# Kernel optimization log

Hardware: AMD Instinct MI355X
Metric: run time of the kernel (lower is better)

## Reference

```python
import jax, jax.numpy as jnp
import numpy as np

HID = 1280
CROSS = 2048
HEAD_DIM = 64
N_HEADS = HID // HEAD_DIM  # 20
FF = 4 * HID               # 5120
EPS = 1e-5


def _layernorm(x, g, b):
    mu = jnp.mean(x, axis=-1, keepdims=True)
    var = jnp.mean(jnp.square(x - mu), axis=-1, keepdims=True)
    return (x - mu) * jax.lax.rsqrt(var + EPS) * g + b


def _attention(x_q, x_kv, wq, wk, wv, wo, bo):
    b, t, _ = x_q.shape
    q = x_q @ wq.T  # [b,t,HID]
    k = x_kv @ wk.T
    v = x_kv @ wv.T
    q = q.reshape(b, t, N_HEADS, HEAD_DIM).transpose(0, 2, 1, 3)
    s = x_kv.shape[1]
    k = k.reshape(b, s, N_HEADS, HEAD_DIM).transpose(0, 2, 1, 3)
    v = v.reshape(b, s, N_HEADS, HEAD_DIM).transpose(0, 2, 1, 3)
    scale = HEAD_DIM ** -0.5
    scores = jnp.einsum('bhtd,bhsd->bhts', q, k) * scale
    attn = jax.nn.softmax(scores, axis=-1)
    o = jnp.einsum('bhts,bhsd->bhtd', attn, v)
    o = o.transpose(0, 2, 1, 3).reshape(b, t, HID)
    return o @ wo.T + bo


def setup_inputs() -> dict:
    key = jax.random.key(0)
    ks = jax.random.split(key, 16)
    std = 0.02
    d = {}
    d['x'] = jax.random.normal(ks[0], (2, 2048, HID), jnp.float32)
    d['encoder_hidden_states'] = jax.random.normal(ks[1], (2, 77, CROSS), jnp.float32)
    d['ln1_g'] = jnp.ones((HID,), jnp.float32); d['ln1_b'] = jnp.zeros((HID,), jnp.float32)
    d['ln2_g'] = jnp.ones((HID,), jnp.float32); d['ln2_b'] = jnp.zeros((HID,), jnp.float32)
    d['ln3_g'] = jnp.ones((HID,), jnp.float32); d['ln3_b'] = jnp.zeros((HID,), jnp.float32)
    d['wq1'] = jax.random.normal(ks[2], (HID, HID), jnp.float32) * std
    d['wk1'] = jax.random.normal(ks[3], (HID, HID), jnp.float32) * std
    d['wv1'] = jax.random.normal(ks[4], (HID, HID), jnp.float32) * std
    d['wo1'] = jax.random.normal(ks[5], (HID, HID), jnp.float32) * std
    d['bo1'] = jnp.zeros((HID,), jnp.float32)
    d['wq2'] = jax.random.normal(ks[6], (HID, HID), jnp.float32) * std
    d['wk2'] = jax.random.normal(ks[7], (HID, CROSS), jnp.float32) * std
    d['wv2'] = jax.random.normal(ks[8], (HID, CROSS), jnp.float32) * std
    d['wo2'] = jax.random.normal(ks[9], (HID, HID), jnp.float32) * std
    d['bo2'] = jnp.zeros((HID,), jnp.float32)
    d['w_geglu'] = jax.random.normal(ks[10], (2 * FF, HID), jnp.float32) * std
    d['b_geglu'] = jnp.zeros((2 * FF,), jnp.float32)
    d['w_ffout'] = jax.random.normal(ks[11], (HID, FF), jnp.float32) * std
    d['b_ffout'] = jnp.zeros((HID,), jnp.float32)
    return d


def reference(x, encoder_hidden_states,
              ln1_g, ln1_b, ln2_g, ln2_b, ln3_g, ln3_b,
              wq1, wk1, wv1, wo1, bo1,
              wq2, wk2, wv2, wo2, bo2,
              w_geglu, b_geglu, w_ffout, b_ffout):
    # self-attention
    h = _layernorm(x, ln1_g, ln1_b)
    x = x + _attention(h, h, wq1, wk1, wv1, wo1, bo1)
    # cross-attention
    h = _layernorm(x, ln2_g, ln2_b)
    x = x + _attention(h, encoder_hidden_states, wq2, wk2, wv2, wo2, bo2)
    # GEGLU feed-forward
    h = _layernorm(x, ln3_g, ln3_b)
    proj = h @ w_geglu.T + b_geglu  # [b,t,2*FF]
    x1, x2 = proj[..., :FF], proj[..., FF:]
    ff = (x1 * jax.nn.gelu(x2, approximate=False)) @ w_ffout.T + b_ffout
    return x + ff
```

## Files before the change

kernel.cpp:

```cpp
#include <hip/hip_runtime.h>

typedef unsigned short u16;
typedef __bf16 bf16x8 __attribute__((ext_vector_type(8)));
typedef float f32x4 __attribute__((ext_vector_type(4)));

#define HID 1280
#define NHEADS 20
#define FFD 5120

__device__ __forceinline__ u16 f2b(float f) {
  union { float f; unsigned u; } a; a.f = f;
  unsigned r = a.u + 0x7FFFu + ((a.u >> 16) & 1u);
  return (u16)(r >> 16);
}

__device__ __forceinline__ float gelu_fast(float x) {
  float z = 1.5957691216f * (x + 0.044715f * x * x * x);
  return x / (1.0f + __expf(-z));
}

__device__ __forceinline__ void g2lds16(const void* g, void* l) {
  __builtin_amdgcn_global_load_lds(
      (__attribute__((address_space(1))) void*)(g),
      (__attribute__((address_space(3))) void*)(l), 16, 0, 0);
}

__device__ __forceinline__ void swz(int& bx, int& by) {
  int nx = gridDim.x, ny = gridDim.y;
  int id = blockIdx.y * nx + blockIdx.x;
  int sx = ((nx & 7) == 0) ? 8 : (((nx & 3) == 0) ? 4 : (((nx & 1) == 0) ? 2 : 1));
  int sy = ((ny & 7) == 0) ? 8 : (((ny & 3) == 0) ? 4 : (((ny & 1) == 0) ? 2 : 1));
  int per = sx * sy;
  int st = id / per, w = id - st * per;
  int nsx = nx / sx;
  int stx = st % nsx, sty = st / nsx;
  bx = stx * sx + (w % sx);
  by = sty * sy + (w / sx);
}

struct CvtArgs {
  const float* src[10];
  u16* dst[10];
  int cum4[11];
};

__global__ __launch_bounds__(256) void cvt_weights(CvtArgs a, int total4) {
  int i = blockIdx.x * 256 + threadIdx.x;
  if (i >= total4) return;
  int seg = 0;
#pragma unroll
  for (int s = 1; s < 10; s++) seg += (i >= a.cum4[s]);
  int j = (i - a.cum4[seg]) * 4;
  float4 f = *(const float4*)(a.src[seg] + j);
  union { unsigned long long u; u16 s[4]; } o;
  o.s[0] = f2b(f.x); o.s[1] = f2b(f.y); o.s[2] = f2b(f.z); o.s[3] = f2b(f.w);
  *(unsigned long long*)(a.dst[seg] + j) = o.u;
}

__global__ __launch_bounds__(256) void cvt_enc(const float* __restrict__ enc,
                                               u16* __restrict__ encp) {
  int i = blockIdx.x * 256 + threadIdx.x;
  int j = i * 4;
  int row = j >> 11;
  unsigned long long out = 0ull;
  if (row < 154) {
    float4 f = *(const float4*)(enc + j);
    union { unsigned long long u; u16 s[4]; } o;
    o.s[0] = f2b(f.x); o.s[1] = f2b(f.y); o.s[2] = f2b(f.z); o.s[3] = f2b(f.w);
    out = o.u;
  }
  *(unsigned long long*)(encp + j) = out;
}

__global__ __launch_bounds__(256) void ln_bf16(const float* __restrict__ X,
                                               const float* __restrict__ g,
                                               const float* __restrict__ bta,
                                               u16* __restrict__ Out) {
  const int row = blockIdx.x, tid = threadIdx.x;
  const float* xr = X + (size_t)row * HID;
  float v[5];
#pragma unroll
  for (int i = 0; i < 5; i++) v[i] = xr[tid + i * 256];
  float s = v[0] + v[1] + v[2] + v[3] + v[4];
#pragma unroll
  for (int off = 32; off >= 1; off >>= 1) s += __shfl_down(s, off);
  __shared__ float red[4];
  if ((tid & 63) == 0) red[tid >> 6] = s;
  __syncthreads();
  float mu = (red[0] + red[1] + red[2] + red[3]) * (1.0f / HID);
  float d = 0.f;
#pragma unroll
  for (int i = 0; i < 5; i++) { float t = v[i] - mu; d += t * t; }
#pragma unroll
  for (int off = 32; off >= 1; off >>= 1) d += __shfl_down(d, off);
  __syncthreads();
  if ((tid & 63) == 0) red[tid >> 6] = d;
  __syncthreads();
  float rstd = rsqrtf((red[0] + red[1] + red[2] + red[3]) * (1.0f / HID) + 1e-5f);
#pragma unroll
  for (int i = 0; i < 5; i++) {
    int c = tid + i * 256;
    Out[(size_t)row * HID + c] = f2b((v[i] - mu) * rstd * g[c] + bta[c]);
  }
}

__global__ __launch_bounds__(256) void gemm_bt(
    const u16* __restrict__ A, const u16* __restrict__ Bw,
    u16* __restrict__ Cb, float* __restrict__ Cf,
    const float* __restrict__ bias, const float* __restrict__ resid,
    int M, int N, int K, int mode, int nsplit) {
  __shared__ u16 As[8192];
  __shared__ u16 Bs[8192];
  const int tid = threadIdx.x;
  const int wid = tid >> 6, lane = tid & 63;
  const int quad = lane >> 4, l16 = lane & 15;
  int bx, by; swz(bx, by);
  const int bm = by * 128, bn = bx * 128;
  const int wm = (wid & 1) * 64, wn = (wid >> 1) * 64;

  size_t aoff[4], boff[4];
#pragma unroll
  for (int c = 0; c < 4; ++c) {
    int g = c * 256 + tid;
    int row = g >> 3, pg = g & 7;
    int sc = (pg ^ (row & 7)) * 8;
    aoff[c] = (size_t)(bm + row) * K + sc;
    boff[c] = (size_t)(bn + row) * K + sc;
  }

  f32x4 acc[4][4] = {};
  const int s7 = l16 & 7;

  for (int k0 = 0; k0 < K; k0 += 64) {
    __syncthreads();
#pragma unroll
    for (int c = 0; c < 4; ++c) {
      g2lds16(A + aoff[c] + k0, &As[(c * 256 + wid * 64) * 8]);
      g2lds16(Bw + boff[c] + k0, &Bs[(c * 256 + wid * 64) * 8]);
    }
    __syncthreads();
#pragma unroll
    for (int kc = 0; kc < 2; kc++) {
      const int ph = ((kc << 2) + quad) ^ s7;
      bf16x8 af[4], bfr[4];
#pragma unroll
      for (int mt = 0; mt < 4; mt++)
        af[mt] = *(const bf16x8*)&As[(wm + mt * 16 + l16) * 64 + ph * 8];
#pragma unroll
      for (int nt = 0; nt < 4; nt++)
        bfr[nt] = *(const bf16x8*)&Bs[(wn + nt * 16 + l16) * 64 + ph * 8];
#pragma unroll
      for (int mt = 0; mt < 4; mt++)
#pragma unroll
        for (int nt = 0; nt < 4; nt++)
          acc[mt][nt] = __builtin_amdgcn_mfma_f32_16x16x32_bf16(af[mt], bfr[nt], acc[mt][nt], 0, 0, 0);
    }
  }

  if (mode == 0) {
#pragma unroll
    for (int mt = 0; mt < 4; mt++)
#pragma unroll
      for (int nt = 0; nt < 4; nt++)
#pragma unroll
        for (int r = 0; r < 4; r++) {
          int row = bm + wm + mt * 16 + quad * 4 + r;
          int col = bn + wn + nt * 16 + l16;
          u16 val = f2b(acc[mt][nt][r]);
          if (nsplit > 0) {
            int t = (col >= 2 * nsplit) ? 2 : ((col >= nsplit) ? 1 : 0);
            int dc = col - t * nsplit;
            Cb[(size_t)t * M * nsplit + (size_t)row * nsplit + dc] = val;
          } else {
            Cb[(size_t)row * N + col] = val;
          }
        }
  } else {
#pragma unroll
    for (int mt = 0; mt < 4; mt++)
#pragma unroll
      for (int nt = 0; nt < 4; nt++)
#pragma unroll
        for (int r = 0; r < 4; r++) {
          int row = bm + wm + mt * 16 + quad * 4 + r;
          int col = bn + wn + nt * 16 + l16;
          size_t idx = (size_t)row * N + col;
          Cf[idx] = acc[mt][nt][r] + bias[col] + resid[idx];
        }
  }
}

__global__ __launch_bounds__(256) void gemm_geglu(
    const u16* __restrict__ A, const u16* __restrict__ W,
    const float* __restrict__ bias, u16* __restrict__ Out,
    int M, int K) {
  __shared__ u16 As[8192];
  __shared__ u16 B1s[4096];
  __shared__ u16 B2s[4096];
  const int tid = threadIdx.x;
  const int wid = tid >> 6, lane = tid & 63;
  const int quad = lane >> 4, l16 = lane & 15;
  int bx, by; swz(bx, by);
  const int bm = by * 128, bn = bx * 64;
  const int wm = (wid & 1) * 64, wn = (wid >> 1) * 32;

  size_t aoff[4], b1off[2], b2off[2];
#pragma unroll
  for (int c = 0; c < 4; ++c) {
    int g = c * 256 + tid;
    int row = g >> 3, pg = g & 7;
    int sc = (pg ^ (row & 7)) * 8;
    aoff[c] = (size_t)(bm + row) * K + sc;
    if (c < 2) {
      b1off[c] = (size_t)(bn + row) * K + sc;
      b2off[c] = (size_t)(FFD + bn + row) * K + sc;
    }
  }

  f32x4 acc1[4][2] = {};
  f32x4 acc2[4][2] = {};
  const int s7 = l16 & 7;

  for (int k0 = 0; k0 < K; k0 += 64) {
    __syncthreads();
#pragma unroll
    for (int c = 0; c < 4; ++c)
      g2lds16(A + aoff[c] + k0, &As[(c * 256 + wid * 64) * 8]);
#pragma unroll
    for (int c = 0; c < 2; ++c) {
      g2lds16(W + b1off[c] + k0, &B1s[(c * 256 + wid * 64) * 8]);
      g2lds16(W + b2off[c] + k0, &B2s[(c * 256 + wid * 64) * 8]);
    }
    __syncthreads();
#pragma unroll
    for (int kc = 0; kc < 2; kc++) {
      const int ph = ((kc << 2) + quad) ^ s7;
      bf16x8 af[4], b1[2], b2[2];
#pragma unroll
      for (int mt = 0; mt < 4; mt++)
        af[mt] = *(const bf16x8*)&As[(wm + mt * 16 + l16) * 64 + ph * 8];
#pragma unroll
      for (int nt = 0; nt < 2; nt++) {
        b1[nt] = *(const bf16x8*)&B1s[(wn + nt * 16 + l16) * 64 + ph * 8];
        b2[nt] = *(const bf16x8*)&B2s[(wn + nt * 16 + l16) * 64 + ph * 8];
      }
#pragma unroll
      for (int mt = 0; mt < 4; mt++)
#pragma unroll
        for (int nt = 0; nt < 2; nt++) {
          acc1[mt][nt] = __builtin_amdgcn_mfma_f32_16x16x32_bf16(af[mt], b1[nt], acc1[mt][nt], 0, 0, 0);
          acc2[mt][nt] = __builtin_amdgcn_mfma_f32_16x16x32_bf16(af[mt], b2[nt], acc2[mt][nt], 0, 0, 0);
        }
    }
  }

#pragma unroll
  for (int mt = 0; mt < 4; mt++)
#pragma unroll
    for (int nt = 0; nt < 2; nt++)
#pragma unroll
      for (int r = 0; r < 4; r++) {
        int row = bm + wm + mt * 16 + quad * 4 + r;
        int col = bn + wn + nt * 16 + l16;
        float v1 = acc1[mt][nt][r] + bias[col];
        float v2 = acc2[mt][nt][r] + bias[FFD + col];
        Out[(size_t)row * FFD + col] = f2b(v1 * gelu_fast(v2));
      }
}

#define BS 128
__global__ __launch_bounds__(256) void flash_attn(
    const u16* __restrict__ Q, const u16* __restrict__ Kb,
    const u16* __restrict__ Vb, u16* __restrict__ O,
    int T, int Sv, float scale) {
  __shared__ u16 Ks[BS * 64];
  __shared__ u16 Vt[64 * BS];
  __shared__ u16 Ps[4][16 * BS];
  const int tid = threadIdx.x, wid = tid >> 6, lane = tid & 63;
  const int quad = lane >> 4, l16 = lane & 15;
  const int b = blockIdx.y / NHEADS, h = blockIdx.y % NHEADS;
  const int q0 = blockIdx.x * 64;

  const size_t qrow = (size_t)(b * T + q0 + wid * 16 + l16);
  bf16x8 aq0 = *(const bf16x8*)&Q[qrow * HID + h * 64 + quad * 8];
  bf16x8 aq1 = *(const bf16x8*)&Q[qrow * HID + h * 64 + 32 + quad * 8];
#pragma unroll
  for (int j = 0; j < 8; j++) {
    aq0[j] = (__bf16)((float)aq0[j] * scale);
    aq1[j] = (__bf16)((float)aq1[j] * scale);
  }
  bf16x8 ones;
#pragma unroll
  for (int j = 0; j < 8; j++) ones[j] = (__bf16)1.0f;

  f32x4 oacc[4] = {};
  float m_i[4], l_i[4];
#pragma unroll
  for (int r = 0; r < 4; r++) { m_i[r] = -1.0e30f; l_i[r] = 0.f; }

  const int ntiles = (Sv + BS - 1) / BS;
  for (int t0 = 0; t0 < ntiles; ++t0) {
    const int srow0 = b * Sv + t0 * BS;
    __syncthreads();
#pragma unroll
    for (int c = 0; c < 4; ++c) {
      int slot = c * 256 + tid;
      int row = slot >> 3, p = slot & 7;
      int gsrc = p ^ (row & 7);
      g2lds16(Kb + (size_t)(srow0 + row) * HID + h * 64 + gsrc * 8,
              &Ks[(size_t)(c * 256 + wid * 64) * 8]);
    }
#pragma unroll
    for (int c = 0; c < 4; ++c) {
      int slot = c * 256 + tid;
      int srow = slot >> 3, scol = (slot & 7) * 8;
      union { uint4 u; u16 e[8]; } vv;
      vv.u = *(const uint4*)&Vb[(size_t)(srow0 + srow) * HID + h * 64 + scol];
      int g = srow >> 3, so = srow & 7;
#pragma unroll
      for (int j = 0; j < 8; j++) {
        int d = scol + j;
        int f = ((d >> 3) ^ d) & 7;
        Vt[d * BS + ((g ^ f) * 8 + so)] = vv.e[j];
      }
    }
    __syncthreads();

    f32x4 sc[8];
#pragma unroll
    for (int nt = 0; nt < 8; nt++) {
      int s = nt * 16 + l16;
      int fb = (s & 7);
      bf16x8 bk0 = *(const bf16x8*)&Ks[s * 64 + ((quad ^ fb) * 8)];
      bf16x8 bk1 = *(const bf16x8*)&Ks[s * 64 + (((quad ^ 4) ^ fb) * 8)];
      f32x4 z = {0.f, 0.f, 0.f, 0.f};
      z = __builtin_amdgcn_mfma_f32_16x16x32_bf16(aq0, bk0, z, 0, 0, 0);
      z = __builtin_amdgcn_mfma_f32_16x16x32_bf16(aq1, bk1, z, 0, 0, 0);
      sc[nt] = z;
    }
    if ((t0 == ntiles - 1) && (Sv & (BS - 1))) {
#pragma unroll
      for (int nt = 0; nt < 8; nt++) {
        int s = t0 * BS + nt * 16 + l16;
        if (s >= Sv)
#pragma unroll
          for (int r = 0; r < 4; r++) sc[nt][r] = -1.0e30f;
      }
    }
    float mnew[4];
#pragma unroll
    for (int r = 0; r < 4; r++) mnew[r] = m_i[r];
#pragma unroll
    for (int nt = 0; nt < 8; nt++)
#pragma unroll
      for (int r = 0; r < 4; r++) mnew[r] = fmaxf(mnew[r], sc[nt][r]);
#pragma unroll
    for (int off = 8; off >= 1; off >>= 1)
#pragma unroll
      for (int r = 0; r < 4; r++) mnew[r] = fmaxf(mnew[r], __shfl_xor(mnew[r], off));

    float alpha[4];
#pragma unroll
    for (int r = 0; r < 4; r++) alpha[r] = __expf(m_i[r] - mnew[r]);
#pragma unroll
    for (int nt = 0; nt < 8; nt++)
#pragma unroll
      for (int r = 0; r < 4; r++) sc[nt][r] = __expf(sc[nt][r] - mnew[r]);

#pragma unroll
    for (int nt = 0; nt < 8; nt++)
#pragma unroll
      for (int r = 0; r < 4; r++) {
        int row = quad * 4 + r, col = nt * 16 + l16;
        int g = col >> 3;
        Ps[wid][row * BS + ((g ^ (row & 7)) * 8 + (col & 7))] = f2b(sc[nt][r]);
      }
    bf16x8 pa[4];
#pragma unroll
    for (int kc = 0; kc < 4; kc++) {
      int lg = kc * 4 + quad;
      pa[kc] = *(const bf16x8*)&Ps[wid][l16 * BS + ((lg ^ (l16 & 7)) * 8)];
    }
    f32x4 ls = {0.f, 0.f, 0.f, 0.f};
#pragma unroll
    for (int kc = 0; kc < 4; kc++)
      ls = __builtin_amdgcn_mfma_f32_16x16x32_bf16(pa[kc], ones, ls, 0, 0, 0);
#pragma unroll
    for (int r = 0; r < 4; r++) {
      l_i[r] = l_i[r] * alpha[r] + ls[r];
      m_i[r] = mnew[r];
    }
#pragma unroll
    for (int dt = 0; dt < 4; dt++)
#pragma unroll
      for (int r = 0; r < 4; r++) oacc[dt][r] *= alpha[r];

#pragma unroll
    for (int dt = 0; dt < 4; dt++) {
      int d = dt * 16 + l16;
      int f = ((d >> 3) ^ d) & 7;
#pragma unroll
      for (int kc = 0; kc < 4; kc++) {
        int lg = kc * 4 + quad;
        bf16x8 bv = *(const bf16x8*)&Vt[d * BS + ((lg ^ f) * 8)];
        oacc[dt] = __builtin_amdgcn_mfma_f32_16x16x32_bf16(pa[kc], bv, oacc[dt], 0, 0, 0);
      }
    }
  }

#pragma unroll
  for (int dt = 0; dt < 4; dt++)
#pragma unroll
    for (int r = 0; r < 4; r++) {
      int row = b * T + q0 + wid * 16 + quad * 4 + r;
      int col = h * 64 + dt * 16 + l16;
      O[(size_t)row * HID + col] = f2b(oacc[dt][r] / l_i[r]);
    }
}

extern "C" void kernel_launch(void* const* d_in, const int* in_sizes, int n_in,
                              void* d_out, int out_size, void* d_ws, size_t ws_size,
                              hipStream_t stream) {
  const float* x    = (const float*)d_in[0];
  const float* enc  = (const float*)d_in[1];
  const float* ln1g = (const float*)d_in[2];
  const float* ln1b = (const float*)d_in[3];
  const float* ln2g = (const float*)d_in[4];
  const float* ln2b = (const float*)d_in[5];
  const float* ln3g = (const float*)d_in[6];
  const float* ln3b = (const float*)d_in[7];
  const float* wq1  = (const float*)d_in[8];
  const float* wk1  = (const float*)d_in[9];
  const float* wv1  = (const float*)d_in[10];
  const float* wo1  = (const float*)d_in[11];
  const float* bo1  = (const float*)d_in[12];
  const float* wq2  = (const float*)d_in[13];
  const float* wk2  = (const float*)d_in[14];
  const float* wv2  = (const float*)d_in[15];
  const float* wo2  = (const float*)d_in[16];
  const float* bo2  = (const float*)d_in[17];
  const float* wg   = (const float*)d_in[18];
  const float* bg   = (const float*)d_in[19];
  const float* wf   = (const float*)d_in[20];
  const float* bfo  = (const float*)d_in[21];
  float* out = (float*)d_out;

  const size_t S1 = 1280 * 1280;
  const size_t S2 = 1280 * 2048;
  const size_t SG = 10240 * 1280;
  const size_t SF = 1280 * 5120;
  const size_t ACT = (size_t)4096 * 1280;

  char* ws = (char*)d_ws;
  size_t off = 0;
  auto alloc = [&](size_t bytes) -> void* {
    void* p = ws + off;
    off += (bytes + 255) & ~(size_t)255;
    return p;
  };
  u16* wq1b = (u16*)alloc(S1 * 2);
  u16* wk1b = (u16*)alloc(S1 * 2);
  u16* wv1b = (u16*)alloc(S1 * 2);
  u16* wo1b = (u16*)alloc(S1 * 2);
  u16* wq2b = (u16*)alloc(S1 * 2);
  u16* wk2b = (u16*)alloc(S2 * 2);
  u16* wv2b = (u16*)alloc(S2 * 2);
  u16* wo2b = (u16*)alloc(S1 * 2);
  u16* wgb  = (u16*)alloc(SG * 2);
  u16* wfb  = (u16*)alloc(SF * 2);
  u16* h    = (u16*)alloc(ACT * 2);
  u16* q    = (u16*)alloc(ACT * 2);
  u16* k    = (u16*)alloc(ACT * 2);
  u16* v    = (u16*)alloc(ACT * 2);
  u16* o    = (u16*)alloc(ACT * 2);
  u16* ffin = q;
  u16* k2   = (u16*)alloc((size_t)256 * 1280 * 2);
  u16* v2   = (u16*)alloc((size_t)256 * 1280 * 2);
  u16* encp = (u16*)alloc((size_t)256 * 2048 * 2);
  float* x2 = out;
  float* x3 = (float*)alloc(ACT * 4);
  (void)k; (void)v; (void)ws_size; (void)in_sizes; (void)n_in; (void)out_size;

  CvtArgs ca;
  const float* srcs[10] = {wq1, wk1, wv1, wo1, wq2, wk2, wv2, wo2, wg, wf};
  u16* dsts[10] = {wq1b, wk1b, wv1b, wo1b, wq2b, wk2b, wv2b, wo2b, wgb, wfb};
  int n4s[10] = {(int)(S1/4), (int)(S1/4), (int)(S1/4), (int)(S1/4), (int)(S1/4),
                 (int)(S2/4), (int)(S2/4), (int)(S1/4), (int)(SG/4), (int)(SF/4)};
  ca.cum4[0] = 0;
  for (int i = 0; i < 10; i++) { ca.src[i] = srcs[i]; ca.dst[i] = dsts[i]; ca.cum4[i+1] = ca.cum4[i] + n4s[i]; }
  int total4 = ca.cum4[10];
  cvt_weights<<<(total4 + 255) / 256, 256, 0, stream>>>(ca, total4);
  cvt_enc<<<512, 256, 0, stream>>>(enc, encp);

  ln_bf16<<<4096, 256, 0, stream>>>(x, ln1g, ln1b, h);
  gemm_bt<<<dim3(30, 32), 256, 0, stream>>>(h, wq1b, q, nullptr, nullptr, nullptr,
                                            4096, 3840, 1280, 0, 1280);
  flash_attn<<<dim3(32, 40), 256, 0, stream>>>(q, k, v, o, 2048, 2048, 0.125f);
  gemm_bt<<<dim3(10, 32), 256, 0, stream>>>(o, wo1b, nullptr, x2, bo1, x,
                                            4096, 1280, 1280, 1, 0);
  ln_bf16<<<4096, 256, 0, stream>>>(x2, ln2g, ln2b, h);
  gemm_bt<<<dim3(10, 32), 256, 0, stream>>>(h, wq2b, q, nullptr, nullptr, nullptr,
                                            4096, 1280, 1280, 0, 0);
  gemm_bt<<<dim3(20, 2), 256, 0, stream>>>(encp, wk2b, k2, nullptr, nullptr, nullptr,
                                           256, 2560, 2048, 0, 1280);
  flash_attn<<<dim3(32, 40), 256, 0, stream>>>(q, k2, v2, o, 2048, 77, 0.125f);
  gemm_bt<<<dim3(10, 32), 256, 0, stream>>>(o, wo2b, nullptr, x3, bo2, x2,
                                            4096, 1280, 1280, 1, 0);
  ln_bf16<<<4096, 256, 0, stream>>>(x3, ln3g, ln3b, h);
  gemm_geglu<<<dim3(80, 32), 256, 0, stream>>>(h, wgb, bg, ffin, 4096, 1280);
  gemm_bt<<<dim3(10, 32), 256, 0, stream>>>(ffin, wfb, nullptr, out, bfo, x3,
                                            4096, 1280, 5120, 1, 0);
}
```

Baseline: 807.1 us.

## Enlarge GEGLU and attention tiles, use exp2 softmax and packed V transpose

The GEGLU GEMM moves to 512-thread blocks covering 256 rows, so each weight tile loaded into LDS is reused by twice as many rows. Flash attention now handles 128 queries per block (two 16-row fragments per wave), halving how often K/V are reloaded and transposed. Softmax switches to exp2 with log2e folded into the Q scale, and the V transpose into LDS uses paired-row 32-bit packed writes instead of scalar 16-bit stores. In exchange, register pressure and LDS use per block go up and fewer blocks are launched, which may lower occupancy.

```diff
diff --git a/kernel.cpp b/kernel.cpp
--- a/kernel.cpp
+++ b/kernel.cpp
@@ -190,31 +190,33 @@
   }
 }
 
-__global__ __launch_bounds__(256) void gemm_geglu(
+__global__ __launch_bounds__(512) void gemm_geglu(
     const u16* __restrict__ A, const u16* __restrict__ W,
     const float* __restrict__ bias, u16* __restrict__ Out,
     int M, int K) {
-  __shared__ u16 As[8192];
-  __shared__ u16 B1s[4096];
-  __shared__ u16 B2s[4096];
+  __shared__ u16 As[256 * 64];
+  __shared__ u16 B1s[64 * 64];
+  __shared__ u16 B2s[64 * 64];
   const int tid = threadIdx.x;
   const int wid = tid >> 6, lane = tid & 63;
   const int quad = lane >> 4, l16 = lane & 15;
   int bx, by; swz(bx, by);
-  const int bm = by * 128, bn = bx * 64;
-  const int wm = (wid & 1) * 64, wn = (wid >> 1) * 32;
-
-  size_t aoff[4], b1off[2], b2off[2];
+  const int bm = by * 256, bn = bx * 64;
+  const int wm = (wid & 3) * 64, wn = (wid >> 2) * 32;
+
+  size_t aoff[4], b1off, b2off;
 #pragma unroll
   for (int c = 0; c < 4; ++c) {
-    int g = c * 256 + tid;
+    int g = c * 512 + tid;
     int row = g >> 3, pg = g & 7;
     int sc = (pg ^ (row & 7)) * 8;
     aoff[c] = (size_t)(bm + row) * K + sc;
-    if (c < 2) {
-      b1off[c] = (size_t)(bn + row) * K + sc;
-      b2off[c] = (size_t)(FFD + bn + row) * K + sc;
-    }
+  }
+  {
+    int row = tid >> 3, pg = tid & 7;
+    int sc = (pg ^ (row & 7)) * 8;
+    b1off = (size_t)(bn + row) * K + sc;
+    b2off = (size_t)(FFD + bn + row) * K + sc;
   }
 
   f32x4 acc1[4][2] = {};
@@ -225,12 +227,9 @@
     __syncthreads();
 #pragma unroll
     for (int c = 0; c < 4; ++c)
-      g2lds16(A + aoff[c] + k0, &As[(c * 256 + wid * 64) * 8]);
-#pragma unroll
-    for (int c = 0; c < 2; ++c) {
-      g2lds16(W + b1off[c] + k0, &B1s[(c * 256 + wid * 64) * 8]);
-      g2lds16(W + b2off[c] + k0, &B2s[(c * 256 + wid * 64) * 8]);
-    }
+      g2lds16(A + aoff[c] + k0, &As[(c * 512 + wid * 64) * 8]);
+    g2lds16(W + b1off + k0, &B1s[(wid * 64) * 8]);
+    g2lds16(W + b2off + k0, &B2s[(wid * 64) * 8]);
     __syncthreads();
 #pragma unroll
     for (int kc = 0; kc < 2; kc++) {
@@ -269,7 +268,7 @@
 }
 
 #define BS 128
-__global__ __launch_bounds__(256) void flash_attn(
+__global__ __launch_bounds__(256, 3) void flash_attn(
     const u16* __restrict__ Q, const u16* __restrict__ Kb,
     const u16* __restrict__ Vb, u16* __restrict__ O,
     int T, int Sv, float scale) {
@@ -279,24 +278,31 @@
   const int tid = threadIdx.x, wid = tid >> 6, lane = tid & 63;
   const int quad = lane >> 4, l16 = lane & 15;
   const int b = blockIdx.y / NHEADS, h = blockIdx.y % NHEADS;
-  const int q0 = blockIdx.x * 64;
-
-  const size_t qrow = (size_t)(b * T + q0 + wid * 16 + l16);
-  bf16x8 aq0 = *(const bf16x8*)&Q[qrow * HID + h * 64 + quad * 8];
-  bf16x8 aq1 = *(const bf16x8*)&Q[qrow * HID + h * 64 + 32 + quad * 8];
-#pragma unroll
-  for (int j = 0; j < 8; j++) {
-    aq0[j] = (__bf16)((float)aq0[j] * scale);
-    aq1[j] = (__bf16)((float)aq1[j] * scale);
+  const int q0 = blockIdx.x * 128;
+  const float lscale = scale * 1.44269504f;
+
+  bf16x8 aq[2][2];
+#pragma unroll
+  for (int f = 0; f < 2; f++) {
+    const size_t qrow = (size_t)(b * T + q0 + wid * 32 + f * 16 + l16);
+    aq[f][0] = *(const bf16x8*)&Q[qrow * HID + h * 64 + quad * 8];
+    aq[f][1] = *(const bf16x8*)&Q[qrow * HID + h * 64 + 32 + quad * 8];
+#pragma unroll
+    for (int j = 0; j < 8; j++) {
+      aq[f][0][j] = (__bf16)((float)aq[f][0][j] * lscale);
+      aq[f][1][j] = (__bf16)((float)aq[f][1][j] * lscale);
+    }
   }
   bf16x8 ones;
 #pragma unroll
   for (int j = 0; j < 8; j++) ones[j] = (__bf16)1.0f;
 
-  f32x4 oacc[4] = {};
-  float m_i[4], l_i[4];
-#pragma unroll
-  for (int r = 0; r < 4; r++) { m_i[r] = -1.0e30f; l_i[r] = 0.f; }
+  f32x4 oacc[2][4] = {};
+  float m_i[2][4], l_i[2][4];
+#pragma unroll
+  for (int f = 0; f < 2; f++)
+#pragma unroll
+    for (int r = 0; r < 4; r++) { m_i[f][r] = -1.0e30f; l_i[f][r] = 0.f; }
 
   const int ntiles = (Sv + BS - 1) / BS;
   for (int t0 = 0; t0 < ntiles; ++t0) {
@@ -313,109 +319,121 @@
 #pragma unroll
     for (int c = 0; c < 4; ++c) {
       int slot = c * 256 + tid;
-      int srow = slot >> 3, scol = (slot & 7) * 8;
-      union { uint4 u; u16 e[8]; } vv;
-      vv.u = *(const uint4*)&Vb[(size_t)(srow0 + srow) * HID + h * 64 + scol];
-      int g = srow >> 3, so = srow & 7;
-#pragma unroll
-      for (int j = 0; j < 8; j++) {
-        int d = scol + j;
-        int f = ((d >> 3) ^ d) & 7;
-        Vt[d * BS + ((g ^ f) * 8 + so)] = vv.e[j];
+      int s2 = (slot >> 4) * 2;
+      int dg = (slot & 15) * 4;
+      const u16* vb = &Vb[(size_t)(srow0 + s2) * HID + h * 64 + dg];
+      uint2 r0 = *(const uint2*)vb;
+      uint2 r1 = *(const uint2*)(vb + HID);
+      unsigned pk[4];
+      pk[0] = (r0.x & 0xFFFFu) | (r1.x << 16);
+      pk[1] = (r0.x >> 16) | (r1.x & 0xFFFF0000u);
+      pk[2] = (r0.y & 0xFFFFu) | (r1.y << 16);
+      pk[3] = (r0.y >> 16) | (r1.y & 0xFFFF0000u);
+      int gsl = s2 >> 3, so = s2 & 7;
+#pragma unroll
+      for (int j = 0; j < 4; j++) {
+        int d = dg + j;
+        int fb = ((d >> 3) ^ d) & 7;
+        *(unsigned*)&Vt[d * BS + ((gsl ^ fb) * 8 + so)] = pk[j];
       }
     }
     __syncthreads();
 
-    f32x4 sc[8];
-#pragma unroll
-    for (int nt = 0; nt < 8; nt++) {
-      int s = nt * 16 + l16;
-      int fb = (s & 7);
-      bf16x8 bk0 = *(const bf16x8*)&Ks[s * 64 + ((quad ^ fb) * 8)];
-      bf16x8 bk1 = *(const bf16x8*)&Ks[s * 64 + (((quad ^ 4) ^ fb) * 8)];
-      f32x4 z = {0.f, 0.f, 0.f, 0.f};
-      z = __builtin_amdgcn_mfma_f32_16x16x32_bf16(aq0, bk0, z, 0, 0, 0);
-      z = __builtin_amdgcn_mfma_f32_16x16x32_bf16(aq1, bk1, z, 0, 0, 0);
-      sc[nt] = z;
-    }
-    if ((t0 == ntiles - 1) && (Sv & (BS - 1))) {
+#pragma unroll
+    for (int f = 0; f < 2; ++f) {
+      f32x4 sc[8];
 #pragma unroll
       for (int nt = 0; nt < 8; nt++) {
-        int s = t0 * BS + nt * 16 + l16;
-        if (s >= Sv)
-#pragma unroll
-          for (int r = 0; r < 4; r++) sc[nt][r] = -1.0e30f;
-      }
-    }
-    float mnew[4];
-#pragma unroll
-    for (int r = 0; r < 4; r++) mnew[r] = m_i[r];
-#pragma unroll
-    for (int nt = 0; nt < 8; nt++)
-#pragma unroll
-      for (int r = 0; r < 4; r++) mnew[r] = fmaxf(mnew[r], sc[nt][r]);
-#pragma unroll
-    for (int off = 8; off >= 1; off >>= 1)
-#pragma unroll
-      for (int r = 0; r < 4; r++) mnew[r] = fmaxf(mnew[r], __shfl_xor(mnew[r], off));
-
-    float alpha[4];
-#pragma unroll
-    for (int r = 0; r < 4; r++) alpha[r] = __expf(m_i[r] - mnew[r]);
-#pragma unroll
-    for (int nt = 0; nt < 8; nt++)
-#pragma unroll
-      for (int r = 0; r < 4; r++) sc[nt][r] = __expf(sc[nt][r] - mnew[r]);
-
-#pragma unroll
-    for (int nt = 0; nt < 8; nt++)
-#pragma unroll
-      for (int r = 0; r < 4; r++) {
-        int row = quad * 4 + r, col = nt * 16 + l16;
-        int g = col >> 3;
-        Ps[wid][row * BS + ((g ^ (row & 7)) * 8 + (col & 7))] = f2b(sc[nt][r]);
-      }
-    bf16x8 pa[4];
-#pragma unroll
-    for (int kc = 0; kc < 4; kc++) {
-      int lg = kc * 4 + quad;
-      pa[kc] = *(const bf16x8*)&Ps[wid][l16 * BS + ((lg ^ (l16 & 7)) * 8)];
-    }
-    f32x4 ls = {0.f, 0.f, 0.f, 0.f};
-#pragma unroll
-    for (int kc = 0; kc < 4; kc++)
-      ls = __builtin_amdgcn_mfma_f32_16x16x32_bf16(pa[kc], ones, ls, 0, 0, 0);
-#pragma unroll
-    for (int r = 0; r < 4; r++) {
-      l_i[r] = l_i[r] * alpha[r] + ls[r];
-      m_i[r] = mnew[r];
-    }
-#pragma unroll
-    for (int dt = 0; dt < 4; dt++)
-#pragma unroll
-      for (int r = 0; r < 4; r++) oacc[dt][r] *= alpha[r];
-
-#pragma unroll
-    for (int dt = 0; dt < 4; dt++) {
-      int d = dt * 16 + l16;
-      int f = ((d >> 3) ^ d) & 7;
+        int s = nt * 16 + l16;
+        int fb = (s & 7);
+        bf16x8 bk0 = *(const bf16x8*)&Ks[s * 64 + ((quad ^ fb) * 8)];
+        bf16x8 bk1 = *(const bf16x8*)&Ks[s * 64 + (((quad ^ 4) ^ fb) * 8)];
+        f32x4 z = {0.f, 0.f, 0.f, 0.f};
+        z = __builtin_amdgcn_mfma_f32_16x16x32_bf16(aq[f][0], bk0, z, 0, 0, 0);
+        z = __builtin_amdgcn_mfma_f32_16x16x32_bf16(aq[f][1], bk1, z, 0, 0, 0);
+        sc[nt] = z;
+      }
+      if ((t0 == ntiles - 1) && (Sv & (BS - 1))) {
+#pragma unroll
+        for (int nt = 0; nt < 8; nt++) {
+          int s = t0 * BS + nt * 16 + l16;
+          if (s >= Sv)
+#pragma unroll
+            for (int r = 0; r < 4; r++) sc[nt][r] = -1.0e30f;
+        }
+      }
+      float mnew[4];
+#pragma unroll
+      for (int r = 0; r < 4; r++) mnew[r] = m_i[f][r];
+#pragma unroll
+      for (int nt = 0; nt < 8; nt++)
+#pragma unroll
+        for (int r = 0; r < 4; r++) mnew[r] = fmaxf(mnew[r], sc[nt][r]);
+#pragma unroll
+      for (int off = 8; off >= 1; off >>= 1)
+#pragma unroll
+        for (int r = 0; r < 4; r++) mnew[r] = fmaxf(mnew[r], __shfl_xor(mnew[r], off));
+
+      float alpha[4];
+#pragma unroll
+      for (int r = 0; r < 4; r++) alpha[r] = exp2f(m_i[f][r] - mnew[r]);
+#pragma unroll
+      for (int nt = 0; nt < 8; nt++)
+#pragma unroll
+        for (int r = 0; r < 4; r++) sc[nt][r] = exp2f(sc[nt][r] - mnew[r]);
+
+#pragma unroll
+      for (int nt = 0; nt < 8; nt++)
+#pragma unroll
+        for (int r = 0; r < 4; r++) {
+          int row = quad * 4 + r, col = nt * 16 + l16;
+          int g = col >> 3;
+          Ps[wid][row * BS + ((g ^ (row & 7)) * 8 + (col & 7))] = f2b(sc[nt][r]);
+        }
+      bf16x8 pa[4];
 #pragma unroll
       for (int kc = 0; kc < 4; kc++) {
         int lg = kc * 4 + quad;
-        bf16x8 bv = *(const bf16x8*)&Vt[d * BS + ((lg ^ f) * 8)];
-        oacc[dt] = __builtin_amdgcn_mfma_f32_16x16x32_bf16(pa[kc], bv, oacc[dt], 0, 0, 0);
-      }
-    }
-  }
-
-#pragma unroll
-  for (int dt = 0; dt < 4; dt++)
-#pragma unroll
-    for (int r = 0; r < 4; r++) {
-      int row = b * T + q0 + wid * 16 + quad * 4 + r;
-      int col = h * 64 + dt * 16 + l16;
-      O[(size_t)row * HID + col] = f2b(oacc[dt][r] / l_i[r]);
-    }
+        pa[kc] = *(const bf16x8*)&Ps[wid][l16 * BS + ((lg ^ (l16 & 7)) * 8)];
+      }
+      f32x4 ls = {0.f, 0.f, 0.f, 0.f};
+#pragma unroll
+      for (int kc = 0; kc < 4; kc++)
+        ls = __builtin_amdgcn_mfma_f32_16x16x32_bf16(pa[kc], ones, ls, 0, 0, 0);
+#pragma unroll
+      for (int r = 0; r < 4; r++) {
+        l_i[f][r] = l_i[f][r] * alpha[r] + ls[r];
+        m_i[f][r] = mnew[r];
+      }
+#pragma unroll
+      for (int dt = 0; dt < 4; dt++)
+#pragma unroll
+        for (int r = 0; r < 4; r++) oacc[f][dt][r] *= alpha[r];
+
+#pragma unroll
+      for (int dt = 0; dt < 4; dt++) {
+        int d = dt * 16 + l16;
+        int fb = ((d >> 3) ^ d) & 7;
+#pragma unroll
+        for (int kc = 0; kc < 4; kc++) {
+          int lg = kc * 4 + quad;
+          bf16x8 bv = *(const bf16x8*)&Vt[d * BS + ((lg ^ fb) * 8)];
+          oacc[f][dt] = __builtin_amdgcn_mfma_f32_16x16x32_bf16(pa[kc], bv, oacc[f][dt], 0, 0, 0);
+        }
+      }
+    }
+  }
+
+#pragma unroll
+  for (int f = 0; f < 2; f++)
+#pragma unroll
+    for (int dt = 0; dt < 4; dt++)
+#pragma unroll
+      for (int r = 0; r < 4; r++) {
+        int row = b * T + q0 + wid * 32 + f * 16 + quad * 4 + r;
+        int col = h * 64 + dt * 16 + l16;
+        O[(size_t)row * HID + col] = f2b(oacc[f][dt][r] / l_i[f][r]);
+      }
 }
 
 extern "C" void kernel_launch(void* const* d_in, const int* in_sizes, int n_in,
@@ -495,7 +513,7 @@
   ln_bf16<<<4096, 256, 0, stream>>>(x, ln1g, ln1b, h);
   gemm_bt<<<dim3(30, 32), 256, 0, stream>>>(h, wq1b, q, nullptr, nullptr, nullptr,
                                             4096, 3840, 1280, 0, 1280);
-  flash_attn<<<dim3(32, 40), 256, 0, stream>>>(q, k, v, o, 2048, 2048, 0.125f);
+  flash_attn<<<dim3(16, 40), 256, 0, stream>>>(q, k, v, o, 2048, 2048, 0.125f);
   gemm_bt<<<dim3(10, 32), 256, 0, stream>>>(o, wo1b, nullptr, x2, bo1, x,
                                             4096, 1280, 1280, 1, 0);
   ln_bf16<<<4096, 256, 0, stream>>>(x2, ln2g, ln2b, h);
@@ -503,11 +521,11 @@
                                             4096, 1280, 1280, 0, 0);
   gemm_bt<<<dim3(20, 2), 256, 0, stream>>>(encp, wk2b, k2, nullptr, nullptr, nullptr,
                                            256, 2560, 2048, 0, 1280);
-  flash_attn<<<dim3(32, 40), 256, 0, stream>>>(q, k2, v2, o, 2048, 77, 0.125f);
+  flash_attn<<<dim3(16, 40), 256, 0, stream>>>(q, k2, v2, o, 2048, 77, 0.125f);
   gemm_bt<<<dim3(10, 32), 256, 0, stream>>>(o, wo2b, nullptr, x3, bo2, x2,
                                             4096, 1280, 1280, 1, 0);
   ln_bf16<<<4096, 256, 0, stream>>>(x3, ln3g, ln3b, h);
-  gemm_geglu<<<dim3(80, 32), 256, 0, stream>>>(h, wgb, bg, ffin, 4096, 1280);
+  gemm_geglu<<<dim3(80, 16), 512, 0, stream>>>(h, wgb, bg, ffin, 4096, 1280);
   gemm_bt<<<dim3(10, 32), 256, 0, stream>>>(ffin, wfb, nullptr, out, bfo, x3,
                                             4096, 1280, 5120, 1, 0);
 }
```

After: 926.1 us. +14.7%, slower.
